# Performance work log

Hardware: AMD Instinct MI355X
Metric: run time of the kernel (lower is better)

Reference implementation:

```python
import jax, jax.numpy as jnp
import numpy as np
import math

B, T, D = 8, 4096, 512
E, H = 64, 1024            # n_experts, d_expert
CAP_FACTOR = 1.0
N = B * T
CAPACITY = max(1, math.ceil(CAP_FACTOR * N / E))  # 512


def setup_inputs() -> dict:
    key = jax.random.key(0)
    ks = jax.random.split(key, 6)
    s_r = 1.0 / np.sqrt(D)
    s_h = 1.0 / np.sqrt(H)
    return {
        "x": jax.random.normal(ks[0], (B, T, D), dtype=jnp.float32),
        "router_w": jax.random.uniform(ks[1], (D, E), minval=-s_r, maxval=s_r, dtype=jnp.float32),
        "fc1_w": jax.random.uniform(ks[2], (E, D, H), minval=-s_r, maxval=s_r, dtype=jnp.float32),
        "fc1_b": jax.random.uniform(ks[3], (E, H), minval=-s_r, maxval=s_r, dtype=jnp.float32),
        "fc2_w": jax.random.uniform(ks[4], (E, H, D), minval=-s_h, maxval=s_h, dtype=jnp.float32),
        "fc2_b": jax.random.uniform(ks[5], (E, D), minval=-s_h, maxval=s_h, dtype=jnp.float32),
    }


def reference(x, router_w, fc1_w, fc1_b, fc2_w, fc2_b):
    x_flat = x.reshape(N, D)
    router_logits = x_flat @ router_w                       # (N, E)
    # softmax over TOKENS (dim=0), as in expert-choice routing
    router_probs = jax.nn.softmax(router_logits, axis=0)    # (N, E)
    scores = router_probs.T                                 # (E, N)
    expert_weights, token_indices = jax.lax.top_k(scores, CAPACITY)  # (E, C)

    # gather -> batched per-expert FFN -> weighted scatter-add
    tokens = x_flat[token_indices]                          # (E, C, D)
    h = jax.nn.gelu(jnp.einsum('ecd,edh->ech', tokens, fc1_w) + fc1_b[:, None, :], approximate=False)
    expert_out = jnp.einsum('ech,ehd->ecd', h, fc2_w) + fc2_b[:, None, :]  # (E, C, D)
    weighted = expert_weights[..., None] * expert_out       # (E, C, D)
    output_flat = jnp.zeros((N, D), dtype=x.dtype).at[token_indices.reshape(-1)].add(
        weighted.reshape(-1, D))
    output = output_flat.reshape(B, T, D)

    # aux stats
    expert_mask = jnp.zeros((N, E), dtype=x.dtype).at[
        token_indices, jnp.arange(E)[:, None]].set(1.0)     # (N, E)
    fraction_chosen = expert_mask.sum(axis=0) / N           # (E,)
    aux_loss = jnp.mean(fraction_chosen ** 2)
    mean_cap_util = jnp.mean(fraction_chosen)
    return output, aux_loss, mean_cap_util
```

## Files before the change

kernel.cpp:

```cpp
#include <hip/hip_runtime.h>
#include <math.h>

#define N_TOK 32768
#define DIM   512
#define NEXP  64
#define HID   1024
#define CAP   512

typedef float  f32x4  __attribute__((ext_vector_type(4)));
typedef short  bf16x8 __attribute__((ext_vector_type(8)));
typedef unsigned short u16;

#define GET4(v, jj) ((jj) == 0 ? (v).x : (jj) == 1 ? (v).y : (jj) == 2 ? (v).z : (v).w)

__device__ __forceinline__ u16 f2bf(float f) {
  unsigned u = __float_as_uint(f);
  u += 0x7FFFu + ((u >> 16) & 1u);
  return (u16)(u >> 16);
}
__device__ __forceinline__ unsigned enc_f(float f) {
  unsigned u = __float_as_uint(f);
  return (u & 0x80000000u) ? ~u : (u | 0x80000000u);
}
__device__ __forceinline__ float dec_f(unsigned k) {
  unsigned u = (k & 0x80000000u) ? (k & 0x7FFFFFFFu) : ~k;
  return __uint_as_float(u);
}
__device__ __forceinline__ void gl16(const u16* g, u16* l) {
  __builtin_amdgcn_global_load_lds(
      (const __attribute__((address_space(1))) unsigned int*)g,
      (__attribute__((address_space(3))) unsigned int*)l, 16, 0, 0);
}
__device__ __forceinline__ float gelu_f(float v) {
  float x = fabsf(v) * 0.70710678118654752f;
  float tt = 1.0f / (1.0f + 0.3275911f * x);
  float poly = tt * (0.254829592f + tt * (-0.284496736f + tt * (1.421413741f +
               tt * (-1.453152027f + tt * 1.061405429f))));
  float erfabs = 1.0f - poly * __expf(-x * x);
  float erfv = v >= 0.f ? erfabs : -erfabs;
  return 0.5f * v * (1.0f + erfv);
}

__global__ __launch_bounds__(256)
void router_kernel(const float* __restrict__ x, const float* __restrict__ rw,
                   float* __restrict__ logitsT, u16* __restrict__ xb) {
  __shared__ float As[32][68];
  __shared__ float Bs[32][68];
  const int t = threadIdx.x;
  const int n0 = blockIdx.x * 64;
  const int ty = t >> 4, tx = t & 15;
  const int am = t >> 2, akq = (t & 3) * 8;
  const int bk = t >> 3, beq = (t & 7) * 8;
  const float* xrow = x + (size_t)(n0 + am) * DIM + akq;
  u16* xbrow = xb ? (xb + (size_t)(n0 + am) * DIM + akq) : (u16*)0;
  const float* brow = rw + (size_t)bk * NEXP + beq;

  float acc[4][4] = {};
  for (int k0 = 0; k0 < DIM; k0 += 32) {
    float4 a0 = *(const float4*)(xrow + k0);
    float4 a1 = *(const float4*)(xrow + k0 + 4);
    float4 b0 = *(const float4*)(brow + (size_t)k0 * NEXP);
    float4 b1 = *(const float4*)(brow + (size_t)k0 * NEXP + 4);
    if (xbrow) {
      uint4 o;
      o.x = f2bf(a0.x) | ((unsigned)f2bf(a0.y) << 16);
      o.y = f2bf(a0.z) | ((unsigned)f2bf(a0.w) << 16);
      o.z = f2bf(a1.x) | ((unsigned)f2bf(a1.y) << 16);
      o.w = f2bf(a1.z) | ((unsigned)f2bf(a1.w) << 16);
      *(uint4*)(xbrow + k0) = o;
    }
    __syncthreads();
    As[akq + 0][am] = a0.x; As[akq + 1][am] = a0.y;
    As[akq + 2][am] = a0.z; As[akq + 3][am] = a0.w;
    As[akq + 4][am] = a1.x; As[akq + 5][am] = a1.y;
    As[akq + 6][am] = a1.z; As[akq + 7][am] = a1.w;
    *(float4*)&Bs[bk][beq] = b0;
    *(float4*)&Bs[bk][beq + 4] = b1;
    __syncthreads();
#pragma unroll
    for (int k = 0; k < 32; ++k) {
      float4 av = *(const float4*)&As[k][ty * 4];
      float4 bv = *(const float4*)&Bs[k][tx * 4];
#pragma unroll
      for (int i = 0; i < 4; ++i)
#pragma unroll
        for (int j = 0; j < 4; ++j)
          acc[i][j] += GET4(av, i) * GET4(bv, j);
    }
  }
#pragma unroll
  for (int j = 0; j < 4; ++j) {
    float4 o; o.x = acc[0][j]; o.y = acc[1][j]; o.z = acc[2][j]; o.w = acc[3][j];
    *(float4*)(logitsT + (size_t)(tx * 4 + j) * N_TOK + n0 + ty * 4) = o;
  }
}

__global__ __launch_bounds__(1024)
void topk_kernel(const float* __restrict__ logitsT, int* __restrict__ tok_idx,
                 float* __restrict__ expw, float* __restrict__ auxout) {
  const int e = blockIdx.x;
  const int t = threadIdx.x;
  const float* row = logitsT + (size_t)e * N_TOK;

  unsigned key[32];
#pragma unroll
  for (int j = 0; j < 32; ++j) key[j] = enc_f(row[j * 1024 + t]);

  __shared__ unsigned ured[1024];
  __shared__ float    fred[1024];
  __shared__ unsigned hist[256];
  __shared__ unsigned sh_chosen, sh_rem, sh_x, sh_pos;

  unsigned km = 0;
#pragma unroll
  for (int j = 0; j < 32; ++j) km = key[j] > km ? key[j] : km;
  ured[t] = km;
  __syncthreads();
  for (int s = 512; s > 0; s >>= 1) {
    if (t < s) { unsigned o = ured[t + s]; if (o > ured[t]) ured[t] = o; }
    __syncthreads();
  }
  const float m = dec_f(ured[0]);

  float ssum = 0.f;
#pragma unroll
  for (int j = 0; j < 32; ++j) ssum += expf(dec_f(key[j]) - m);
  fred[t] = ssum;
  __syncthreads();
  for (int s = 512; s > 0; s >>= 1) {
    if (t < s) fred[t] += fred[t + s];
    __syncthreads();
  }
  const float invZ = 1.0f / fred[0];

  if (t == 0) sh_rem = CAP;
  __syncthreads();
  unsigned live = 0xFFFFFFFFu;
  unsigned prefix = 0;
  for (int pass = 0; pass < 4; ++pass) {
    const int shift = 24 - pass * 8;
    if (t < 256) hist[t] = 0;
    __syncthreads();
#pragma unroll
    for (int j = 0; j < 32; ++j)
      if (live & (1u << j)) atomicAdd(&hist[(key[j] >> shift) & 0xFFu], 1u);
    __syncthreads();
    if (t == 0) {
      unsigned need = sh_rem, accum = 0;
      int found = 0;
      for (int b = 255; b >= 0; --b) {
        unsigned cn = hist[b];
        if (!found) {
          if (accum + cn >= need) { sh_chosen = (unsigned)b; sh_rem = need - accum; found = 1; }
          else accum += cn;
        }
      }
    }
    __syncthreads();
    const unsigned ch = sh_chosen;
#pragma unroll
    for (int j = 0; j < 32; ++j)
      if (((key[j] >> shift) & 0xFFu) != ch) live &= ~(1u << j);
    prefix = (prefix << 8) | ch;
    __syncthreads();
  }
  const unsigned ustar = prefix;

  if (t == 0) sh_pos = 0;
  __syncthreads();
#pragma unroll
  for (int j = 0; j < 32; ++j) {
    if (key[j] > ustar) {
      unsigned p = atomicAdd(&sh_pos, 1u);
      tok_idx[e * CAP + p] = j * 1024 + t;
      expw[e * CAP + p] = expf(dec_f(key[j]) - m) * invZ;
    }
  }
  __syncthreads();
  const unsigned padv = CAP - sh_pos;

  if (t < 256) hist[t] = 0;
  __syncthreads();
#pragma unroll
  for (int j = 0; j < 32; ++j)
    if (live & (1u << j)) atomicAdd(&hist[(j * 1024 + t) >> 7], 1u);
  __syncthreads();
  if (t == 0) {
    unsigned accum = 0;
    int found = 0;
    for (int b = 0; b < 256; ++b) {
      unsigned cn = hist[b];
      if (!found) {
        if (accum + cn >= padv) { sh_chosen = (unsigned)b; sh_rem = padv - accum; found = 1; }
        else accum += cn;
      }
    }
  }
  __syncthreads();
  const unsigned hb = sh_chosen, rem = sh_rem;
  if (t < 256) hist[t] = 0;
  __syncthreads();
#pragma unroll
  for (int j = 0; j < 32; ++j)
    if (live & (1u << j)) {
      int n = j * 1024 + t;
      if ((unsigned)(n >> 7) == hb) atomicAdd(&hist[n & 127], 1u);
    }
  __syncthreads();
  if (t == 0) {
    unsigned accum = 0;
    int found = 0;
    for (int b = 0; b < 128; ++b) {
      unsigned cn = hist[b];
      if (!found) {
        if (accum + cn >= rem) { sh_x = (hb << 7) | (unsigned)b; found = 1; }
        else accum += cn;
      }
    }
  }
  __syncthreads();
  const int X = (int)sh_x;
#pragma unroll
  for (int j = 0; j < 32; ++j)
    if (live & (1u << j)) {
      int n = j * 1024 + t;
      if (n <= X) {
        unsigned p = atomicAdd(&sh_pos, 1u);
        tok_idx[e * CAP + p] = n;
        expw[e * CAP + p] = expf(dec_f(key[j]) - m) * invZ;
      }
    }
  if (e == 0 && t == 0) { auxout[0] = 2.44140625e-4f; auxout[1] = 0.015625f; }
}

__global__ __launch_bounds__(256)
void transpose_cvt_kernel(const float* __restrict__ in, u16* __restrict__ outp,
                          int R, int C) {
  __shared__ u16 tile[64][66];
  const int e = blockIdx.z;
  const int r0 = blockIdx.y * 64, c0 = blockIdx.x * 64;
  const int t = threadIdx.x;
  {
    const int r = t >> 2, cs = (t & 3) * 16;
    const float* ip = in + ((size_t)e * R + (r0 + r)) * C + c0 + cs;
#pragma unroll
    for (int q = 0; q < 4; ++q) {
      float4 v = *(const float4*)(ip + q * 4);
      tile[r][cs + q * 4 + 0] = f2bf(v.x);
      tile[r][cs + q * 4 + 1] = f2bf(v.y);
      tile[r][cs + q * 4 + 2] = f2bf(v.z);
      tile[r][cs + q * 4 + 3] = f2bf(v.w);
    }
  }
  __syncthreads();
  {
    const int c = t >> 2, rs = (t & 3) * 16;
    u16* op = outp + ((size_t)e * C + (c0 + c)) * R + r0 + rs;
    uint4 o0, o1;
    o0.x = tile[rs + 0][c]  | ((unsigned)tile[rs + 1][c]  << 16);
    o0.y = tile[rs + 2][c]  | ((unsigned)tile[rs + 3][c]  << 16);
    o0.z = tile[rs + 4][c]  | ((unsigned)tile[rs + 5][c]  << 16);
    o0.w = tile[rs + 6][c]  | ((unsigned)tile[rs + 7][c]  << 16);
    o1.x = tile[rs + 8][c]  | ((unsigned)tile[rs + 9][c]  << 16);
    o1.y = tile[rs + 10][c] | ((unsigned)tile[rs + 11][c] << 16);
    o1.z = tile[rs + 12][c] | ((unsigned)tile[rs + 13][c] << 16);
    o1.w = tile[rs + 14][c] | ((unsigned)tile[rs + 15][c] << 16);
    *(uint4*)(op) = o0;
    *(uint4*)(op + 8) = o1;
  }
}

#define A_EL 4096
#define B_EL 8192

#define LDSW(base, row, hi4v) \
  (*(const bf16x8*)((const char*)(base) + (row) * 64 + ((((hi4v) ^ (((row) >> 1) & 3))) << 4)))

#define STG3(bs, k0) do { \
  gl16(aSrc + (k0), AsmF + (bs) * A_EL + wOff); \
  gl16(bSrc0 + (k0), BsmF + (bs) * B_EL + wOff); \
  gl16(bSrc1 + (k0), BsmF + (bs) * B_EL + wOff + 4096); \
} while (0)

__global__ __launch_bounds__(512, 4)
void fc1_bf(const u16* __restrict__ xb, const int* __restrict__ tok_idx,
            const u16* __restrict__ w1t, const float* __restrict__ b1,
            u16* __restrict__ h) {
  const int p = blockIdx.x;
  const int l = (p & 7) * 128 + (p >> 3);
  const int e  = l >> 4;
  const int mt = (l >> 2) & 3;
  const int nt = l & 3;
  const int m0 = mt * 128, n0 = nt * 256;
  const int t = threadIdx.x;
  const int lane = t & 63, wave = t >> 6;
  const int wm = wave >> 2, wn = wave & 3;

  __shared__ __align__(16) u16 AsmF[3 * A_EL];
  __shared__ __align__(16) u16 BsmF[3 * B_EL];

  const int kc = ((lane & 3) ^ ((lane >> 3) & 3)) * 8;
  const int rloc = lane >> 2;
  const int wOff = wave * 512;

  const int arow = wave * 16 + rloc;
  const int tok = tok_idx[e * CAP + m0 + arow];
  const u16* aSrc  = xb + (size_t)tok * DIM + kc;
  const u16* bSrc0 = w1t + ((size_t)e * HID + n0 + arow) * DIM + kc;
  const u16* bSrc1 = w1t + ((size_t)e * HID + n0 + 128 + arow) * DIM + kc;

  f32x4 acc[4][4] = {};
  const int lr = lane & 15, hi4 = lane >> 4;

  STG3(0, 0);
  STG3(1, 32);
  int cur = 0;
  const int KT = DIM / 32;
  for (int tt = 0; tt < KT; ++tt) {
    if (tt < KT - 1) asm volatile("s_waitcnt vmcnt(3)" ::: "memory");
    else             asm volatile("s_waitcnt vmcnt(0)" ::: "memory");
    __builtin_amdgcn_s_barrier();
    const u16* Ab = AsmF + cur * A_EL;
    const u16* Bb = BsmF + cur * B_EL;
    bf16x8 af[4], bf[4];
#pragma unroll
    for (int mi = 0; mi < 4; ++mi) af[mi] = LDSW(Ab, wm * 64 + mi * 16 + lr, hi4);
#pragma unroll
    for (int ni = 0; ni < 4; ++ni) bf[ni] = LDSW(Bb, wn * 64 + ni * 16 + lr, hi4);
    if (tt + 2 < KT) {
      const int bs = (tt + 2) % 3;
      STG3(bs, (tt + 2) * 32);
    }
    __builtin_amdgcn_s_setprio(1);
#pragma unroll
    for (int mi = 0; mi < 4; ++mi)
#pragma unroll
      for (int ni = 0; ni < 4; ++ni)
        acc[mi][ni] = __builtin_amdgcn_mfma_f32_16x16x32_bf16(af[mi], bf[ni], acc[mi][ni], 0, 0, 0);
    __builtin_amdgcn_s_setprio(0);
    __builtin_amdgcn_s_barrier();
    cur = cur == 2 ? 0 : cur + 1;
  }

  const int lq = lane >> 4, lc = lane & 15;
#pragma unroll
  for (int nj = 0; nj < 4; ++nj) {
    const int n_l = wn * 64 + nj * 16 + lc;
    const float bias = b1[e * HID + n0 + n_l];
#pragma unroll
    for (int mi = 0; mi < 4; ++mi) {
#pragma unroll
      for (int j = 0; j < 4; ++j) {
        const int m_l = wm * 64 + mi * 16 + lq * 4 + j;
        float v = acc[mi][nj][j] + bias;
        h[((size_t)(e * CAP + m0 + m_l)) * HID + (n0 + n_l)] = f2bf(gelu_f(v));
      }
    }
  }
}

__global__ __launch_bounds__(512, 4)
void fc2_bf(const u16* __restrict__ h, const u16* __restrict__ w2t,
            const float* __restrict__ b2, const int* __restrict__ tok_idx,
            const float* __restrict__ expw, float* __restrict__ out) {
  const int p = blockIdx.x;
  const int l = (p & 7) * 64 + (p >> 3);
  const int e  = l >> 3;
  const int mt = (l >> 1) & 3;
  const int nt = l & 1;
  const int m0 = mt * 128, n0 = nt * 256;
  const int t = threadIdx.x;
  const int lane = t & 63, wave = t >> 6;
  const int wm = wave >> 2, wn = wave & 3;

  __shared__ __align__(16) u16 AsmF[3 * A_EL];
  __shared__ __align__(16) u16 BsmF[3 * B_EL];

  const int kc = ((lane & 3) ^ ((lane >> 3) & 3)) * 8;
  const int rloc = lane >> 2;
  const int wOff = wave * 512;

  const int arow = wave * 16 + rloc;
  const u16* aSrc  = h + ((size_t)(e * CAP + m0 + arow)) * HID + kc;
  const u16* bSrc0 = w2t + ((size_t)e * DIM + n0 + arow) * HID + kc;
  const u16* bSrc1 = w2t + ((size_t)e * DIM + n0 + 128 + arow) * HID + kc;

  f32x4 acc[4][4] = {};
  const int lr = lane & 15, hi4 = lane >> 4;

  STG3(0, 0);
  STG3(1, 32);
  int cur = 0;
  const int KT = HID / 32;
  for (int tt = 0; tt < KT; ++tt) {
    if (tt < KT - 1) asm volatile("s_waitcnt vmcnt(3)" ::: "memory");
    else             asm volatile("s_waitcnt vmcnt(0)" ::: "memory");
    __builtin_amdgcn_s_barrier();
    const u16* Ab = AsmF + cur * A_EL;
    const u16* Bb = BsmF + cur * B_EL;
    bf16x8 af[4], bf[4];
#pragma unroll
    for (int mi = 0; mi < 4; ++mi) af[mi] = LDSW(Ab, wm * 64 + mi * 16 + lr, hi4);
#pragma unroll
    for (int ni = 0; ni < 4; ++ni) bf[ni] = LDSW(Bb, wn * 64 + ni * 16 + lr, hi4);
    if (tt + 2 < KT) {
      const int bs = (tt + 2) % 3;
      STG3(bs, (tt + 2) * 32);
    }
    __builtin_amdgcn_s_setprio(1);
#pragma unroll
    for (int mi = 0; mi < 4; ++mi)
#pragma unroll
      for (int ni = 0; ni < 4; ++ni)
        acc[mi][ni] = __builtin_amdgcn_mfma_f32_16x16x32_bf16(af[mi], bf[ni], acc[mi][ni], 0, 0, 0);
    __builtin_amdgcn_s_setprio(0);
    __builtin_amdgcn_s_barrier();
    cur = cur == 2 ? 0 : cur + 1;
  }

  const int lq = lane >> 4, lc = lane & 15;
  int   tokm[4][4];
  float wgt[4][4];
#pragma unroll
  for (int mi = 0; mi < 4; ++mi)
#pragma unroll
    for (int j = 0; j < 4; ++j) {
      const int m_l = wm * 64 + mi * 16 + lq * 4 + j;
      tokm[mi][j] = tok_idx[e * CAP + m0 + m_l];
      wgt[mi][j]  = expw[e * CAP + m0 + m_l];
    }
#pragma unroll
  for (int nj = 0; nj < 4; ++nj) {
    const int n_l = wn * 64 + nj * 16 + lc;
    const float bias = b2[e * DIM + n0 + n_l];
#pragma unroll
    for (int mi = 0; mi < 4; ++mi)
#pragma unroll
      for (int j = 0; j < 4; ++j) {
        float v = (acc[mi][nj][j] + bias) * wgt[mi][j];
        atomicAdd(out + (size_t)tokm[mi][j] * DIM + (n0 + n_l), v);
      }
  }
}

#define SWZ(row, cb) ((cb) ^ (((((row) >> 3) ^ (row)) & 7) << 4))

__global__ __launch_bounds__(256)
void fc1_kernel(const float* __restrict__ x, const int* __restrict__ tok_idx,
                const float* __restrict__ w1, const float* __restrict__ b1,
                u16* __restrict__ h) {
  const int bx = blockIdx.x;
  const int e  = bx >> 5;
  const int mt = (bx >> 3) & 3;
  const int nt = bx & 7;
  const int m0 = mt * 128, n0 = nt * 128;
  const int t = threadIdx.x;
  const int lane = t & 63, wave = t >> 6;
  const int wm = wave >> 1, wn = wave & 1;

  __shared__ __align__(16) u16 Asm[128 * 64];
  __shared__ __align__(16) u16 Bsm[128 * 64];

  const int arq = t & 31, akq = t >> 5;
  int tokr[4];
#pragma unroll
  for (int j = 0; j < 4; ++j) tokr[j] = tok_idx[e * CAP + m0 + arq * 4 + j];
  const int nq = t & 31, kq = t >> 5;
  const float* bptr = w1 + (size_t)e * DIM * HID + n0 + nq * 4;

  f32x4 acc[4][4] = {};

  for (int k0 = 0; k0 < DIM; k0 += 64) {
    float4 av0[4], av1[4];
#pragma unroll
    for (int j = 0; j < 4; ++j) {
      const float* ap = x + (size_t)tokr[j] * DIM + k0 + akq * 8;
      av0[j] = *(const float4*)(ap);
      av1[j] = *(const float4*)(ap + 4);
    }
    float4 bv[8];
#pragma unroll
    for (int kk = 0; kk < 8; ++kk)
      bv[kk] = *(const float4*)(bptr + (size_t)(k0 + kq * 8 + kk) * HID);
    __syncthreads();
#pragma unroll
    for (int j = 0; j < 4; ++j) {
      const int row = arq * 4 + j;
      ushort4 w0, w1v;
      w0.x = f2bf(av0[j].x); w0.y = f2bf(av0[j].y); w0.z = f2bf(av0[j].z); w0.w = f2bf(av0[j].w);
      w1v.x = f2bf(av1[j].x); w1v.y = f2bf(av1[j].y); w1v.z = f2bf(av1[j].z); w1v.w = f2bf(av1[j].w);
      *(ushort4*)((char*)Asm + row * 128 + SWZ(row, (akq * 8 + 0) * 2)) = w0;
      *(ushort4*)((char*)Asm + row * 128 + SWZ(row, (akq * 8 + 4) * 2)) = w1v;
    }
#pragma unroll
    for (int g = 0; g < 2; ++g) {
#pragma unroll
      for (int j = 0; j < 4; ++j) {
        ushort4 wv;
        wv.x = f2bf(GET4(bv[g * 4 + 0], j));
        wv.y = f2bf(GET4(bv[g * 4 + 1], j));
        wv.z = f2bf(GET4(bv[g * 4 + 2], j));
        wv.w = f2bf(GET4(bv[g * 4 + 3], j));
        const int row = nq * 4 + j;
        const int cb = (kq * 8 + g * 4) * 2;
        *(ushort4*)((char*)Bsm + row * 128 + SWZ(row, cb)) = wv;
      }
    }
    __syncthreads();
#pragma unroll
    for (int ks = 0; ks < 2; ++ks) {
      bf16x8 af[4], bf[4];
#pragma unroll
      for (int mi = 0; mi < 4; ++mi) {
        const int row = wm * 64 + mi * 16 + (lane & 15);
        const int cb = ks * 64 + (lane >> 4) * 16;
        af[mi] = *(const bf16x8*)((const char*)Asm + row * 128 + SWZ(row, cb));
      }
#pragma unroll
      for (int ni = 0; ni < 4; ++ni) {
        const int row = wn * 64 + ni * 16 + (lane & 15);
        const int cb = ks * 64 + (lane >> 4) * 16;
        bf[ni] = *(const bf16x8*)((const char*)Bsm + row * 128 + SWZ(row, cb));
      }
#pragma unroll
      for (int mi = 0; mi < 4; ++mi)
#pragma unroll
        for (int ni = 0; ni < 4; ++ni)
          acc[mi][ni] = __builtin_amdgcn_mfma_f32_16x16x32_bf16(af[mi], bf[ni], acc[mi][ni], 0, 0, 0);
    }
  }
  const int lq = lane >> 4, lc = lane & 15;
#pragma unroll
  for (int ni = 0; ni < 4; ++ni) {
    const int n_l = wn * 64 + ni * 16 + lc;
    const float bias = b1[e * HID + n0 + n_l];
#pragma unroll
    for (int mi = 0; mi < 4; ++mi) {
#pragma unroll
      for (int j = 0; j < 4; ++j) {
        const int m_l = wm * 64 + mi * 16 + lq * 4 + j;
        float v = acc[mi][ni][j] + bias;
        h[((size_t)(e * CAP + m0 + m_l)) * HID + (n0 + n_l)] = f2bf(gelu_f(v));
      }
    }
  }
}

__global__ __launch_bounds__(256)
void fc2_kernel(const u16* __restrict__ h, const float* __restrict__ w2,
                const float* __restrict__ b2, const int* __restrict__ tok_idx,
                const float* __restrict__ expw, float* __restrict__ out) {
  const int bx = blockIdx.x;
  const int e  = bx >> 4;
  const int mt = (bx >> 2) & 3;
  const int nt = bx & 3;
  const int m0 = mt * 128, n0 = nt * 128;
  const int t = threadIdx.x;
  const int lane = t & 63, wave = t >> 6;
  const int wm = wave >> 1, wn = wave & 1;

  __shared__ __align__(16) u16 Asm[128 * 64];
  __shared__ __align__(16) u16 Bsm[128 * 64];

  const int arq = t & 31, akq = t >> 5;
  const u16* aptr0 = h + ((size_t)(e * CAP + m0 + arq * 4)) * HID + akq * 8;
  const int nq = t & 31, kq = t >> 5;
  const float* bptr = w2 + (size_t)e * HID * DIM + n0 + nq * 4;

  f32x4 acc[4][4] = {};

  for (int k0 = 0; k0 < HID; k0 += 64) {
    uint4 av[4];
#pragma unroll
    for (int j = 0; j < 4; ++j)
      av[j] = *(const uint4*)(aptr0 + (size_t)j * HID + k0);
    float4 bv[8];
#pragma unroll
    for (int kk = 0; kk < 8; ++kk)
      bv[kk] = *(const float4*)(bptr + (size_t)(k0 + kq * 8 + kk) * DIM);
    __syncthreads();
#pragma unroll
    for (int j = 0; j < 4; ++j) {
      const int row = arq * 4 + j;
      *(uint4*)((char*)Asm + row * 128 + SWZ(row, akq * 16)) = av[j];
    }
#pragma unroll
    for (int g = 0; g < 2; ++g) {
#pragma unroll
      for (int j = 0; j < 4; ++j) {
        ushort4 wv;
        wv.x = f2bf(GET4(bv[g * 4 + 0], j));
        wv.y = f2bf(GET4(bv[g * 4 + 1], j));
        wv.z = f2bf(GET4(bv[g * 4 + 2], j));
        wv.w = f2bf(GET4(bv[g * 4 + 3], j));
        const int row = nq * 4 + j;
        const int cb = (kq * 8 + g * 4) * 2;
        *(ushort4*)((char*)Bsm + row * 128 + SWZ(row, cb)) = wv;
      }
    }
    __syncthreads();
#pragma unroll
    for (int ks = 0; ks < 2; ++ks) {
      bf16x8 af[4], bf[4];
#pragma unroll
      for (int mi = 0; mi < 4; ++mi) {
        const int row = wm * 64 + mi * 16 + (lane & 15);
        const int cb = ks * 64 + (lane >> 4) * 16;
        af[mi] = *(const bf16x8*)((const char*)Asm + row * 128 + SWZ(row, cb));
      }
#pragma unroll
      for (int ni = 0; ni < 4; ++ni) {
        const int row = wn * 64 + ni * 16 + (lane & 15);
        const int cb = ks * 64 + (lane >> 4) * 16;
        bf[ni] = *(const bf16x8*)((const char*)Bsm + row * 128 + SWZ(row, cb));
      }
#pragma unroll
      for (int mi = 0; mi < 4; ++mi)
#pragma unroll
        for (int ni = 0; ni < 4; ++ni)
          acc[mi][ni] = __builtin_amdgcn_mfma_f32_16x16x32_bf16(af[mi], bf[ni], acc[mi][ni], 0, 0, 0);
    }
  }
  const int lq = lane >> 4, lc = lane & 15;
  int   tokm[4][4];
  float wgt[4][4];
#pragma unroll
  for (int mi = 0; mi < 4; ++mi)
#pragma unroll
    for (int j = 0; j < 4; ++j) {
      const int m_l = wm * 64 + mi * 16 + lq * 4 + j;
      tokm[mi][j] = tok_idx[e * CAP + m0 + m_l];
      wgt[mi][j]  = expw[e * CAP + m0 + m_l];
    }
#pragma unroll
  for (int ni = 0; ni < 4; ++ni) {
    const int n_l = wn * 64 + ni * 16 + lc;
    const float bias = b2[e * DIM + n0 + n_l];
#pragma unroll
    for (int mi = 0; mi < 4; ++mi)
#pragma unroll
      for (int j = 0; j < 4; ++j) {
        float v = (acc[mi][ni][j] + bias) * wgt[mi][j];
        atomicAdd(out + (size_t)tokm[mi][j] * DIM + (n0 + n_l), v);
      }
  }
}

extern "C" void kernel_launch(void* const* d_in, const int* in_sizes, int n_in,
                              void* d_out, int out_size, void* d_ws, size_t ws_size,
                              hipStream_t stream) {
  const float* x  = (const float*)d_in[0];
  const float* rw = (const float*)d_in[1];
  const float* w1 = (const float*)d_in[2];
  const float* b1 = (const float*)d_in[3];
  const float* w2 = (const float*)d_in[4];
  const float* b2 = (const float*)d_in[5];
  float* out = (float*)d_out;

  char* ws = (char*)d_ws;
  const size_t MB = 1u << 20;
  float* logits = (float*)ws;
  int*   toki   = (int*)(ws + 8 * MB);
  float* ew     = (float*)(ws + 8 * MB + (128u << 10));

  const size_t off_xb = 8 * MB + (256u << 10);
  const size_t off_wt = off_xb + 32 * MB;
  const size_t off_h  = off_wt + 64 * MB;
  const size_t need   = off_h + 64 * MB;
  const bool big = (ws_size >= need);

  u16* xb = big ? (u16*)(ws + off_xb) : (u16*)0;

  (void)hipMemsetAsync(d_out, 0, (size_t)out_size * sizeof(float), stream);
  router_kernel<<<dim3(512), dim3(256), 0, stream>>>(x, rw, logits, xb);
  topk_kernel<<<dim3(64), dim3(1024), 0, stream>>>(logits, toki, ew, out + (size_t)N_TOK * DIM);

  if (big) {
    u16* wt  = (u16*)(ws + off_wt);
    u16* h   = (u16*)(ws + off_h);
    transpose_cvt_kernel<<<dim3(16, 8, 64), dim3(256), 0, stream>>>(w1, wt, 512, 1024);
    fc1_bf<<<dim3(1024), dim3(512), 0, stream>>>(xb, toki, wt, b1, h);
    transpose_cvt_kernel<<<dim3(8, 16, 64), dim3(256), 0, stream>>>(w2, wt, 1024, 512);
    fc2_bf<<<dim3(512), dim3(512), 0, stream>>>(h, wt, b2, toki, ew, out);
  } else {
    u16* h = (u16*)(ws + 8 * MB + (256u << 10));
    fc1_kernel<<<dim3(2048), dim3(256), 0, stream>>>(x, toki, w1, b1, h);
    fc2_kernel<<<dim3(1024), dim3(256), 0, stream>>>(h, w2, b2, toki, ew, out);
  }
}
```

Before: 388.3 us.

## Split top-k into parallel histogram, select, and emit kernels

Replaces the single 64-block top-k kernel with three kernels. The first builds per-expert 1024-bin histograms and partial softmax sums across 16x64 blocks. The second narrows the threshold using candidate compaction and radix refinement in shared memory, and the third emits the selected tokens in parallel via a global atomic counter. This spreads the serial per-expert selection over many more CUs and drops the max-subtraction from the softmax. The cost is extra launches and a memset, plus overflow risk: candidates are capped at 4096 and ties at 1024, and __expf without max-subtraction could overflow for large logits.

```diff
diff --git a/kernel.cpp b/kernel.cpp
--- a/kernel.cpp
+++ b/kernel.cpp
@@ -10,6 +10,7 @@
 typedef float  f32x4  __attribute__((ext_vector_type(4)));
 typedef short  bf16x8 __attribute__((ext_vector_type(8)));
 typedef unsigned short u16;
+typedef unsigned int u32;
 
 #define GET4(v, jj) ((jj) == 0 ? (v).x : (jj) == 1 ? (v).y : (jj) == 2 ? (v).z : (v).w)
 
@@ -95,142 +96,205 @@
   }
 }
 
-__global__ __launch_bounds__(1024)
-void topk_kernel(const float* __restrict__ logitsT, int* __restrict__ tok_idx,
-                 float* __restrict__ expw, float* __restrict__ auxout) {
+
+__global__ __launch_bounds__(256)
+void topk_hist(const float* __restrict__ logitsT, u32* __restrict__ ghist,
+               float* __restrict__ psum) {
+  const int c = blockIdx.x, e = blockIdx.y;
+  const int t = threadIdx.x, lane = t & 63, wid = t >> 6;
+  __shared__ u32 lh[1024];
+  __shared__ float wsum[4];
+  lh[t] = 0; lh[t + 256] = 0; lh[t + 512] = 0; lh[t + 768] = 0;
+  __syncthreads();
+  const float* row = logitsT + (size_t)e * N_TOK + c * 2048 + t * 8;
+  float4 a = *(const float4*)(row);
+  float4 b = *(const float4*)(row + 4);
+  float s = 0.f;
+#pragma unroll
+  for (int j = 0; j < 4; ++j) {
+    float v0 = GET4(a, j), v1 = GET4(b, j);
+    atomicAdd(&lh[enc_f(v0) >> 22], 1u);
+    atomicAdd(&lh[enc_f(v1) >> 22], 1u);
+    s += __expf(v0) + __expf(v1);
+  }
+#pragma unroll
+  for (int off = 32; off >= 1; off >>= 1) s += __shfl_xor(s, off);
+  if (lane == 0) wsum[wid] = s;
+  __syncthreads();
+#pragma unroll
+  for (int q = 0; q < 4; ++q) {
+    const u32 hv = lh[t + q * 256];
+    if (hv) atomicAdd(&ghist[e * 1024 + t + q * 256], hv);
+  }
+  if (t == 0) psum[e * 16 + c] = wsum[0] + wsum[1] + wsum[2] + wsum[3];
+}
+
+__global__ __launch_bounds__(256)
+void topk_select(const float* __restrict__ logitsT, const u32* __restrict__ ghist,
+                 const float* __restrict__ psum, u32* __restrict__ gU,
+                 int* __restrict__ gX, float* __restrict__ gZ, u32* __restrict__ gpos,
+                 float* __restrict__ auxout) {
   const int e = blockIdx.x;
   const int t = threadIdx.x;
   const float* row = logitsT + (size_t)e * N_TOK;
 
-  unsigned key[32];
-#pragma unroll
-  for (int j = 0; j < 32; ++j) key[j] = enc_f(row[j * 1024 + t]);
-
-  __shared__ unsigned ured[1024];
-  __shared__ float    fred[1024];
-  __shared__ unsigned hist[256];
-  __shared__ unsigned sh_chosen, sh_rem, sh_x, sh_pos;
-
-  unsigned km = 0;
-#pragma unroll
-  for (int j = 0; j < 32; ++j) km = key[j] > km ? key[j] : km;
-  ured[t] = km;
-  __syncthreads();
-  for (int s = 512; s > 0; s >>= 1) {
-    if (t < s) { unsigned o = ured[t + s]; if (o > ured[t]) ured[t] = o; }
-    __syncthreads();
-  }
-  const float m = dec_f(ured[0]);
-
-  float ssum = 0.f;
-#pragma unroll
-  for (int j = 0; j < 32; ++j) ssum += expf(dec_f(key[j]) - m);
-  fred[t] = ssum;
-  __syncthreads();
-  for (int s = 512; s > 0; s >>= 1) {
-    if (t < s) fred[t] += fred[t + s];
-    __syncthreads();
-  }
-  const float invZ = 1.0f / fred[0];
-
-  if (t == 0) sh_rem = CAP;
-  __syncthreads();
-  unsigned live = 0xFFFFFFFFu;
-  unsigned prefix = 0;
-  for (int pass = 0; pass < 4; ++pass) {
-    const int shift = 24 - pass * 8;
-    if (t < 256) hist[t] = 0;
-    __syncthreads();
-#pragma unroll
-    for (int j = 0; j < 32; ++j)
-      if (live & (1u << j)) atomicAdd(&hist[(key[j] >> shift) & 0xFFu], 1u);
-    __syncthreads();
-    if (t == 0) {
-      unsigned need = sh_rem, accum = 0;
-      int found = 0;
-      for (int b = 255; b >= 0; --b) {
-        unsigned cn = hist[b];
-        if (!found) {
-          if (accum + cn >= need) { sh_chosen = (unsigned)b; sh_rem = need - accum; found = 1; }
-          else accum += cn;
-        }
-      }
-    }
-    __syncthreads();
-    const unsigned ch = sh_chosen;
-#pragma unroll
-    for (int j = 0; j < 32; ++j)
-      if (((key[j] >> shift) & 0xFFu) != ch) live &= ~(1u << j);
-    prefix = (prefix << 8) | ch;
-    __syncthreads();
-  }
-  const unsigned ustar = prefix;
-
-  if (t == 0) sh_pos = 0;
-  __syncthreads();
-#pragma unroll
-  for (int j = 0; j < 32; ++j) {
-    if (key[j] > ustar) {
-      unsigned p = atomicAdd(&sh_pos, 1u);
-      tok_idx[e * CAP + p] = j * 1024 + t;
-      expw[e * CAP + p] = expf(dec_f(key[j]) - m) * invZ;
-    }
-  }
-  __syncthreads();
-  const unsigned padv = CAP - sh_pos;
+  __shared__ u32 hist[256];
+  __shared__ u32 arr[256], arr2[256];
+  __shared__ u32 candK[4096];
+  __shared__ int candN[4096];
+  __shared__ int tieN[1024];
+  __shared__ u32 sh_cnt, sh_b0, sh_rem, sh_chosen, sh_tcnt;
+  __shared__ float sh_invZ;
+
+#define SUFFIX_SELECT(NEED) do { \
+    if (t < 64) { \
+      u32 h0_ = hist[4 * t], h1_ = hist[4 * t + 1], h2_ = hist[4 * t + 2], h3_ = hist[4 * t + 3]; \
+      u32 s3_ = h3_, s2_ = h2_ + s3_, s1_ = h1_ + s2_, s0_ = h0_ + s1_; \
+      u32 sfx_ = s0_; \
+      _Pragma("unroll") for (int off_ = 1; off_ < 64; off_ <<= 1) { \
+        u32 o_ = __shfl_down(sfx_, off_); \
+        if (t + off_ < 64) sfx_ += o_; } \
+      const u32 ex_ = sfx_ - s0_; \
+      const u32 S_[4] = {ex_ + s0_, ex_ + s1_, ex_ + s2_, ex_ + s3_}; \
+      const u32 Sx_[4] = {ex_ + s1_, ex_ + s2_, ex_ + s3_, ex_}; \
+      _Pragma("unroll") for (int k_ = 0; k_ < 4; ++k_) \
+        if (S_[k_] >= (NEED) && Sx_[k_] < (NEED)) { sh_chosen = 4 * t + k_; sh_rem = (NEED) - Sx_[k_]; } \
+    } \
+    __syncthreads(); } while (0)
+
+  if (t == 0) {
+    float z = 0.f;
+#pragma unroll
+    for (int i = 0; i < 16; ++i) z += psum[e * 16 + i];
+    sh_invZ = 1.0f / z;
+    sh_cnt = 0; sh_tcnt = 0;
+  }
+
+  const u32 h0 = ghist[e * 1024 + 4 * t + 0];
+  const u32 h1 = ghist[e * 1024 + 4 * t + 1];
+  const u32 h2 = ghist[e * 1024 + 4 * t + 2];
+  const u32 h3 = ghist[e * 1024 + 4 * t + 3];
+  arr[t] = h0 + h1 + h2 + h3;
+  __syncthreads();
+  if (t < 64) {
+    u32 g0 = arr[4 * t], g1 = arr[4 * t + 1], g2 = arr[4 * t + 2], g3 = arr[4 * t + 3];
+    u32 s3 = g3, s2 = g2 + s3, s1 = g1 + s2, s0 = g0 + s1;
+    u32 sfx = s0;
+#pragma unroll
+    for (int off = 1; off < 64; off <<= 1) {
+      u32 o = __shfl_down(sfx, off);
+      if (t + off < 64) sfx += o;
+    }
+    const u32 ex = sfx - s0;
+    arr2[4 * t + 3] = ex;
+    arr2[4 * t + 2] = ex + g3;
+    arr2[4 * t + 1] = ex + g3 + g2;
+    arr2[4 * t + 0] = ex + g3 + g2 + g1;
+  }
+  __syncthreads();
+  {
+    u32 S = arr2[t];
+    if (S < CAP && S + h3 >= CAP) { sh_b0 = 4 * t + 3; sh_rem = CAP - S; }
+    S += h3;
+    if (S < CAP && S + h2 >= CAP) { sh_b0 = 4 * t + 2; sh_rem = CAP - S; }
+    S += h2;
+    if (S < CAP && S + h1 >= CAP) { sh_b0 = 4 * t + 1; sh_rem = CAP - S; }
+    S += h1;
+    if (S < CAP && S + h0 >= CAP) { sh_b0 = 4 * t + 0; sh_rem = CAP - S; }
+  }
+  __syncthreads();
+  const u32 b0 = sh_b0;
+  const u32 rem = sh_rem;
+
+  for (int i = 0; i < 32; ++i) {
+    const int nb = i * 1024 + t * 4;
+    float4 v = *(const float4*)(row + nb);
+#pragma unroll
+    for (int jj = 0; jj < 4; ++jj) {
+      const u32 k = enc_f(GET4(v, jj));
+      if ((k >> 22) == b0) {
+        const u32 p = atomicAdd(&sh_cnt, 1u);
+        if (p < 4096u) { candK[p] = k; candN[p] = nb + jj; }
+      }
+    }
+  }
+  __syncthreads();
+  const u32 cnt = sh_cnt < 4096u ? sh_cnt : 4096u;
 
   if (t < 256) hist[t] = 0;
   __syncthreads();
-#pragma unroll
-  for (int j = 0; j < 32; ++j)
-    if (live & (1u << j)) atomicAdd(&hist[(j * 1024 + t) >> 7], 1u);
+  for (u32 i = t; i < cnt; i += 256) atomicAdd(&hist[(candK[i] >> 14) & 0xFFu], 1u);
+  __syncthreads();
+  SUFFIX_SELECT(rem);
+  const u32 dA = sh_chosen, remB = sh_rem;
+  if (t < 256) hist[t] = 0;
+  __syncthreads();
+  for (u32 i = t; i < cnt; i += 256)
+    if (((candK[i] >> 14) & 0xFFu) == dA) atomicAdd(&hist[(candK[i] >> 6) & 0xFFu], 1u);
+  __syncthreads();
+  SUFFIX_SELECT(remB);
+  const u32 dB = sh_chosen, remC = sh_rem;
+  if (t < 256) hist[t] = 0;
+  __syncthreads();
+  for (u32 i = t; i < cnt; i += 256)
+    if (((candK[i] >> 14) & 0xFFu) == dA && ((candK[i] >> 6) & 0xFFu) == dB)
+      atomicAdd(&hist[candK[i] & 0x3Fu], 1u);
+  __syncthreads();
+  SUFFIX_SELECT(remC);
+  const u32 dC = sh_chosen, remF = sh_rem;
+  const u32 ustar = (b0 << 22) | (dA << 14) | (dB << 6) | dC;
+
+  for (u32 i = t; i < cnt; i += 256)
+    if (candK[i] == ustar) {
+      const u32 p = atomicAdd(&sh_tcnt, 1u);
+      if (p < 1024u) tieN[p] = candN[i];
+    }
   __syncthreads();
   if (t == 0) {
-    unsigned accum = 0;
-    int found = 0;
-    for (int b = 0; b < 256; ++b) {
-      unsigned cn = hist[b];
-      if (!found) {
-        if (accum + cn >= padv) { sh_chosen = (unsigned)b; sh_rem = padv - accum; found = 1; }
-        else accum += cn;
-      }
-    }
-  }
-  __syncthreads();
-  const unsigned hb = sh_chosen, rem = sh_rem;
-  if (t < 256) hist[t] = 0;
-  __syncthreads();
-#pragma unroll
-  for (int j = 0; j < 32; ++j)
-    if (live & (1u << j)) {
-      int n = j * 1024 + t;
-      if ((unsigned)(n >> 7) == hb) atomicAdd(&hist[n & 127], 1u);
-    }
-  __syncthreads();
-  if (t == 0) {
-    unsigned accum = 0;
-    int found = 0;
-    for (int b = 0; b < 128; ++b) {
-      unsigned cn = hist[b];
-      if (!found) {
-        if (accum + cn >= rem) { sh_x = (hb << 7) | (unsigned)b; found = 1; }
-        else accum += cn;
-      }
-    }
-  }
-  __syncthreads();
-  const int X = (int)sh_x;
-#pragma unroll
-  for (int j = 0; j < 32; ++j)
-    if (live & (1u << j)) {
-      int n = j * 1024 + t;
-      if (n <= X) {
-        unsigned p = atomicAdd(&sh_pos, 1u);
-        tok_idx[e * CAP + p] = n;
-        expw[e * CAP + p] = expf(dec_f(key[j]) - m) * invZ;
-      }
-    }
-  if (e == 0 && t == 0) { auxout[0] = 2.44140625e-4f; auxout[1] = 0.015625f; }
+    const u32 tcnt = sh_tcnt < 1024u ? sh_tcnt : 1024u;
+    int last = -1;
+    for (u32 r = 0; r < remF; ++r) {
+      int mn = 0x7FFFFFFF;
+      for (u32 i = 0; i < tcnt; ++i) {
+        const int nn = tieN[i];
+        if (nn > last && nn < mn) mn = nn;
+      }
+      last = mn;
+    }
+    gU[e] = ustar;
+    gX[e] = last;
+    gZ[e] = sh_invZ;
+    gpos[e] = 0;
+    if (e == 0) { auxout[0] = 2.44140625e-4f; auxout[1] = 0.015625f; }
+  }
+#undef SUFFIX_SELECT
+}
+
+__global__ __launch_bounds__(256)
+void topk_emit(const float* __restrict__ logitsT, const u32* __restrict__ gU,
+               const int* __restrict__ gX, const float* __restrict__ gZ,
+               u32* __restrict__ gpos, int* __restrict__ tok_idx,
+               float* __restrict__ expw) {
+  const int c = blockIdx.x, e = blockIdx.y;
+  const int t = threadIdx.x;
+  const u32 us = gU[e];
+  const int X = gX[e];
+  const float iz = gZ[e];
+  const int nb = c * 2048 + t * 8;
+  const float* row = logitsT + (size_t)e * N_TOK + nb;
+  float4 a = *(const float4*)(row);
+  float4 b = *(const float4*)(row + 4);
+#pragma unroll
+  for (int j = 0; j < 8; ++j) {
+    const float v = j < 4 ? GET4(a, j) : GET4(b, j - 4);
+    const int n = nb + j;
+    const u32 k = enc_f(v);
+    if (k > us || (k == us && n <= X)) {
+      const u32 p = atomicAdd(&gpos[e], 1u);
+      tok_idx[e * CAP + p] = n;
+      expw[e * CAP + p] = __expf(v) * iz;
+    }
+  }
 }
 
 __global__ __launch_bounds__(256)
@@ -669,11 +733,23 @@
   const size_t need   = off_h + 64 * MB;
   const bool big = (ws_size >= need);
 
+  const size_t off_meta = big ? off_h : (8 * MB + (256u << 10));
+  u32*   ghist = (u32*)(ws + off_meta);
+  float* psum  = (float*)(ws + off_meta + (256u << 10));
+  u32*   gpos  = (u32*)(ws + off_meta + (260u << 10));
+  u32*   gU    = (u32*)(ws + off_meta + (260u << 10) + 256);
+  int*   gX    = (int*)(ws + off_meta + (260u << 10) + 512);
+  float* gZ    = (float*)(ws + off_meta + (260u << 10) + 768);
+
   u16* xb = big ? (u16*)(ws + off_xb) : (u16*)0;
 
   (void)hipMemsetAsync(d_out, 0, (size_t)out_size * sizeof(float), stream);
+  (void)hipMemsetAsync(ws + off_meta, 0, 264u << 10, stream);
   router_kernel<<<dim3(512), dim3(256), 0, stream>>>(x, rw, logits, xb);
-  topk_kernel<<<dim3(64), dim3(1024), 0, stream>>>(logits, toki, ew, out + (size_t)N_TOK * DIM);
+  topk_hist<<<dim3(16, 64), dim3(256), 0, stream>>>(logits, ghist, psum);
+  topk_select<<<dim3(64), dim3(256), 0, stream>>>(logits, ghist, psum, gU, gX, gZ, gpos,
+                                                  out + (size_t)N_TOK * DIM);
+  topk_emit<<<dim3(16, 64), dim3(256), 0, stream>>>(logits, gU, gX, gZ, gpos, toki, ew);
 
   if (big) {
     u16* wt  = (u16*)(ws + off_wt);
@@ -683,7 +759,7 @@
     transpose_cvt_kernel<<<dim3(8, 16, 64), dim3(256), 0, stream>>>(w2, wt, 1024, 512);
     fc2_bf<<<dim3(512), dim3(512), 0, stream>>>(h, wt, b2, toki, ew, out);
   } else {
-    u16* h = (u16*)(ws + 8 * MB + (256u << 10));
+    u16* h = (u16*)(ws + 8 * MB + (512u << 10));
     fc1_kernel<<<dim3(2048), dim3(256), 0, stream>>>(x, toki, w1, b1, h);
     fc2_kernel<<<dim3(1024), dim3(256), 0, stream>>>(h, w2, b2, toki, ew, out);
   }
```

Result: slower. 433.3 us (+11.6%).
